# Kernel tuning notes

Measured on AMD Instinct MI355X. Metric: run time of the kernel, lower is better.

Reference implementation:

```python
import jax, jax.numpy as jnp
import numpy as np
from jax import lax

N, H, W, C = 32, 56, 56, 256
K, RATE, STRIDE = 3, 2, 1
BN_EPS = 1e-3  # keras BatchNormalization default epsilon
DN = ('NHWC', 'HWIO', 'NHWC')


def setup_inputs() -> dict:
    key = jax.random.key(0)
    ks = jax.random.split(key, 5)
    return {
        'x': jax.random.normal(ks[0], (N, H, W, C), jnp.float32),
        'dw_kernel': jax.random.normal(ks[1], (K, K, 1, C), jnp.float32) * 0.1,
        'dw_bias': jnp.zeros((C,), jnp.float32),
        'pw_kernel': jax.random.normal(ks[2], (1, 1, C, C), jnp.float32) * 0.05,
        'pw_bias': jnp.zeros((C,), jnp.float32),
        'gamma': jnp.ones((C,), jnp.float32),
        'beta': jnp.zeros((C,), jnp.float32),
        'moving_mean': jax.random.normal(ks[3], (C,), jnp.float32) * 0.1,
        'moving_var': jax.random.uniform(ks[4], (C,), jnp.float32, 0.5, 1.5),
    }


def reference(x, dw_kernel, dw_bias, pw_kernel, pw_bias, gamma, beta, moving_mean, moving_var):
    # ReLU
    h = jax.nn.relu(x)
    # dilated depthwise conv, stride 1, SAME padding (approx-mult LUT modeled as exact MACs)
    h = lax.conv_general_dilated(
        h, dw_kernel, window_strides=(1, 1), padding='SAME',
        rhs_dilation=(RATE, RATE), dimension_numbers=DN,
        feature_group_count=C) + dw_bias
    # pointwise 1x1 conv with stride
    h = lax.conv_general_dilated(
        h, pw_kernel, window_strides=(STRIDE, STRIDE), padding='SAME',
        dimension_numbers=DN) + pw_bias
    # batch norm (inference mode: moving statistics)
    inv = gamma * lax.rsqrt(moving_var + BN_EPS)
    return h * inv + (beta - moving_mean * inv)
```

## Files before the change

kernel.cpp:

```cpp
#include <hip/hip_runtime.h>


typedef _Float16 f16;
typedef _Float16 f16x4 __attribute__((ext_vector_type(4)));
typedef _Float16 f16x8 __attribute__((ext_vector_type(8)));
typedef float    f32x4 __attribute__((ext_vector_type(4)));

constexpr int   N_ = 32, H_ = 56, W_ = 56, C_ = 256;
constexpr int   PIX = 64;
constexpr float BN_EPS = 1e-3f;
constexpr int   WS_BYTES = 4 * 16384 * 2;

struct SM {
    f16   d[PIX * 256];
    f16   w[256 * 64];
    float offC[256];
};

__global__ void prep_w(const float* __restrict__ pwk,
                       const float* __restrict__ gamma,
                       const float* __restrict__ mvar,
                       f16* __restrict__ ws16)
{
    const int co = blockIdx.x;
    const int t  = threadIdx.x;
    const float iv = gamma[co] * rsqrtf(mvar[co] + BN_EPS);
    const float v  = pwk[(size_t)t * C_ + co] * iv;
    const int chunk = t >> 6, k = t & 63;
    ws16[chunk * 16384 + co * 64 + (((k >> 3) ^ (co & 7)) << 3) + (k & 7)] = (f16)v;
}

template <bool FROM_WS>
__global__ __launch_bounds__(256, 2)
void dilconv_mfma(const float* __restrict__ x,
                  const float* __restrict__ dwk,
                  const float* __restrict__ dwb,
                  const float* __restrict__ pwk,
                  const float* __restrict__ pwb,
                  const float* __restrict__ gamma,
                  const float* __restrict__ beta,
                  const float* __restrict__ mmean,
                  const float* __restrict__ mvar,
                  const f16*   __restrict__ wsw,
                  float* __restrict__ out)
{
    extern __shared__ char smem_raw[];
    SM& sm = *reinterpret_cast<SM*>(smem_raw);

    const int tid = threadIdx.x;
    const int bid = (blockIdx.x & 7) * 196 + (blockIdx.x >> 3);
    const int n   = bid / 49;
    const int t   = bid % 49;
    const int h0  = (t / 7) * 8;
    const int w0  = (t % 7) * 8;
    const int l   = tid & 63;
    const int wq  = tid >> 6;

    float invW;
    {
        const float iv = gamma[tid] * rsqrtf(mvar[tid] + BN_EPS);
        invW = iv;
        sm.offC[tid] = pwb[tid] * iv + beta[tid] - mmean[tid] * iv;
    }

    {
        const int c4 = l << 2;
        const int p0 = wq << 4;
        float4 kreg[9];
        #pragma unroll
        for (int kk = 0; kk < 9; ++kk)
            kreg[kk] = *reinterpret_cast<const float4*>(dwk + kk * C_ + c4);
        const float4 bias = *reinterpret_cast<const float4*>(dwb + c4);

        #pragma unroll 2
        for (int pi = 0; pi < 16; ++pi) {
            const int p  = p0 + pi;
            const int ph = h0 + (p >> 3);
            const int pw = w0 + (p & 7);
            float ax = bias.x, ay = bias.y, az = bias.z, aw = bias.w;
            #pragma unroll
            for (int kh = 0; kh < 3; ++kh) {
                const int ih = ph + 2 * kh - 2;
                #pragma unroll
                for (int kw = 0; kw < 3; ++kw) {
                    const int iw = pw + 2 * kw - 2;
                    if ((unsigned)ih < (unsigned)H_ && (unsigned)iw < (unsigned)W_) {
                        const float4 v = *reinterpret_cast<const float4*>(
                            x + (((size_t)(n * H_ + ih) * W_ + iw) * C_) + c4);
                        const float4 kv = kreg[kh * 3 + kw];
                        ax = fmaf(fmaxf(v.x, 0.f), kv.x, ax);
                        ay = fmaf(fmaxf(v.y, 0.f), kv.y, ay);
                        az = fmaf(fmaxf(v.z, 0.f), kv.z, az);
                        aw = fmaf(fmaxf(v.w, 0.f), kv.w, aw);
                    }
                }
            }
            const f16x4 hv = { (f16)ax, (f16)ay, (f16)az, (f16)aw };
            const int idx = p * 256 + ((((c4 >> 3) ^ (p & 7)) << 3) | (c4 & 7));
            *reinterpret_cast<f16x4*>(&sm.d[idx]) = hv;
        }
    }

    f32x4 acc[4][4];
    #pragma unroll
    for (int i = 0; i < 4; ++i)
        #pragma unroll
        for (int j = 0; j < 4; ++j) acc[i][j] = (f32x4){0.f, 0.f, 0.f, 0.f};

    const int arow = l & 15;
    const int koct = l >> 4;

    for (int c = 0; c < 4; ++c) {
        __syncthreads();
        if constexpr (FROM_WS) {
            const float4* wsrc = reinterpret_cast<const float4*>(wsw) + c * 2048;
            #pragma unroll
            for (int i = 0; i < 8; ++i) {
                const int u = i * 256 + tid;
                const float4 v = wsrc[u];
                *reinterpret_cast<float4*>(&sm.w[u * 8]) = v;
            }
        } else {
            const int co = tid;
            const float* wcol = pwk + (size_t)c * 64 * C_ + co;
            #pragma unroll
            for (int g = 0; g < 8; ++g) {
                f16x8 hv;
                #pragma unroll
                for (int j = 0; j < 8; ++j)
                    hv[j] = (f16)(wcol[(g * 8 + j) * C_] * invW);
                *reinterpret_cast<f16x8*>(&sm.w[co * 64 + ((g ^ (co & 7)) << 3)]) = hv;
            }
        }
        __syncthreads();

        #pragma unroll
        for (int ks = 0; ks < 2; ++ks) {
            f16x8 a[4], b[4];
            const int aslot = c * 8 + ks * 4 + koct;
            #pragma unroll
            for (int mt = 0; mt < 4; ++mt) {
                const int row = mt * 16 + arow;
                a[mt] = *reinterpret_cast<const f16x8*>(
                    &sm.d[row * 256 + ((aslot ^ (arow & 7)) << 3)]);
            }
            #pragma unroll
            for (int nt = 0; nt < 4; ++nt) {
                const int co = wq * 64 + nt * 16 + arow;
                b[nt] = *reinterpret_cast<const f16x8*>(
                    &sm.w[co * 64 + (((ks * 4 + koct) ^ (co & 7)) << 3)]);
            }
            #pragma unroll
            for (int mt = 0; mt < 4; ++mt)
                #pragma unroll
                for (int nt = 0; nt < 4; ++nt)
                    acc[mt][nt] = __builtin_amdgcn_mfma_f32_16x16x32_f16(
                        a[mt], b[nt], acc[mt][nt], 0, 0, 0);
        }
    }

    const int prb = (l >> 4) * 4;
    #pragma unroll
    for (int nt = 0; nt < 4; ++nt) {
        const int co  = wq * 64 + nt * 16 + (l & 15);
        const float off = sm.offC[co];
        #pragma unroll
        for (int mt = 0; mt < 4; ++mt) {
            #pragma unroll
            for (int r = 0; r < 4; ++r) {
                const int p  = mt * 16 + prb + r;
                const int oh = h0 + (p >> 3);
                const int ow = w0 + (p & 7);
                out[((size_t)((n * H_ + oh) * W_ + ow)) * C_ + co] = acc[mt][nt][r] + off;
            }
        }
    }
}

extern "C" void kernel_launch(void* const* d_in, const int* in_sizes, int n_in,
                              void* d_out, int out_size, void* d_ws, size_t ws_size,
                              hipStream_t stream) {
    const float* x     = (const float*)d_in[0];
    const float* dwk   = (const float*)d_in[1];
    const float* dwb   = (const float*)d_in[2];
    const float* pwk   = (const float*)d_in[3];
    const float* pwb   = (const float*)d_in[4];
    const float* gam   = (const float*)d_in[5];
    const float* bet   = (const float*)d_in[6];
    const float* mmean = (const float*)d_in[7];
    const float* mvar  = (const float*)d_in[8];
    float* out = (float*)d_out;

    const bool use_ws = (ws_size >= (size_t)WS_BYTES);

    if (use_ws) {
        f16* ws16 = (f16*)d_ws;
        prep_w<<<dim3(256), dim3(256), 0, stream>>>(pwk, gam, mvar, ws16);
        (void)hipFuncSetAttribute(reinterpret_cast<const void*>(&dilconv_mfma<true>),
                                  hipFuncAttributeMaxDynamicSharedMemorySize,
                                  (int)sizeof(SM));
        dilconv_mfma<true><<<dim3(N_ * 49), dim3(256), sizeof(SM), stream>>>(
            x, dwk, dwb, pwk, pwb, gam, bet, mmean, mvar, ws16, out);
    } else {
        (void)hipFuncSetAttribute(reinterpret_cast<const void*>(&dilconv_mfma<false>),
                                  hipFuncAttributeMaxDynamicSharedMemorySize,
                                  (int)sizeof(SM));
        dilconv_mfma<false><<<dim3(N_ * 49), dim3(256), sizeof(SM), stream>>>(
            x, dwk, dwb, pwk, pwb, gam, bet, mmean, mvar, nullptr, out);
    }
}
```

Measured before the change: 347.7 us.

## Restructure fused dilated conv: 512 threads, row-wise depthwise reuse, register-held weights

```diff
diff --git a/kernel.cpp b/kernel.cpp
--- a/kernel.cpp
+++ b/kernel.cpp
@@ -7,171 +7,150 @@
 typedef float    f32x4 __attribute__((ext_vector_type(4)));
 
 constexpr int   N_ = 32, H_ = 56, W_ = 56, C_ = 256;
-constexpr int   PIX = 64;
 constexpr float BN_EPS = 1e-3f;
-constexpr int   WS_BYTES = 4 * 16384 * 2;
 
 struct SM {
-    f16   d[PIX * 256];
-    f16   w[256 * 64];
+    f16   d[64 * 256];
     float offC[256];
 };
 
-__global__ void prep_w(const float* __restrict__ pwk,
-                       const float* __restrict__ gamma,
-                       const float* __restrict__ mvar,
-                       f16* __restrict__ ws16)
+__global__ __launch_bounds__(512, 4)
+void dilconv_fused(const float* __restrict__ x,
+                   const float* __restrict__ dwk,
+                   const float* __restrict__ dwb,
+                   const float* __restrict__ pwk,
+                   const float* __restrict__ pwb,
+                   const float* __restrict__ gamma,
+                   const float* __restrict__ beta,
+                   const float* __restrict__ mmean,
+                   const float* __restrict__ mvar,
+                   float* __restrict__ out)
 {
-    const int co = blockIdx.x;
-    const int t  = threadIdx.x;
-    const float iv = gamma[co] * rsqrtf(mvar[co] + BN_EPS);
-    const float v  = pwk[(size_t)t * C_ + co] * iv;
-    const int chunk = t >> 6, k = t & 63;
-    ws16[chunk * 16384 + co * 64 + (((k >> 3) ^ (co & 7)) << 3) + (k & 7)] = (f16)v;
-}
-
-template <bool FROM_WS>
-__global__ __launch_bounds__(256, 2)
-void dilconv_mfma(const float* __restrict__ x,
-                  const float* __restrict__ dwk,
-                  const float* __restrict__ dwb,
-                  const float* __restrict__ pwk,
-                  const float* __restrict__ pwb,
-                  const float* __restrict__ gamma,
-                  const float* __restrict__ beta,
-                  const float* __restrict__ mmean,
-                  const float* __restrict__ mvar,
-                  const f16*   __restrict__ wsw,
-                  float* __restrict__ out)
-{
-    extern __shared__ char smem_raw[];
-    SM& sm = *reinterpret_cast<SM*>(smem_raw);
+    __shared__ SM sm;
 
     const int tid = threadIdx.x;
+    const int l   = tid & 63;
+    const int wq  = tid >> 6;
     const int bid = (blockIdx.x & 7) * 196 + (blockIdx.x >> 3);
     const int n   = bid / 49;
     const int t   = bid % 49;
     const int h0  = (t / 7) * 8;
     const int w0  = (t % 7) * 8;
-    const int l   = tid & 63;
-    const int wq  = tid >> 6;
 
-    float invW;
-    {
+    if (tid < 256) {
         const float iv = gamma[tid] * rsqrtf(mvar[tid] + BN_EPS);
-        invW = iv;
         sm.offC[tid] = pwb[tid] * iv + beta[tid] - mmean[tid] * iv;
     }
 
     {
+        const int r  = wq;
         const int c4 = l << 2;
-        const int p0 = wq << 4;
-        float4 kreg[9];
+        const int ph = h0 + r;
+        float4 a[8];
+        const float4 bias = *reinterpret_cast<const float4*>(dwb + c4);
         #pragma unroll
-        for (int kk = 0; kk < 9; ++kk)
-            kreg[kk] = *reinterpret_cast<const float4*>(dwk + kk * C_ + c4);
-        const float4 bias = *reinterpret_cast<const float4*>(dwb + c4);
+        for (int ow = 0; ow < 8; ++ow) a[ow] = bias;
 
-        #pragma unroll 2
-        for (int pi = 0; pi < 16; ++pi) {
-            const int p  = p0 + pi;
-            const int ph = h0 + (p >> 3);
-            const int pw = w0 + (p & 7);
-            float ax = bias.x, ay = bias.y, az = bias.z, aw = bias.w;
+        #pragma unroll
+        for (int kh = 0; kh < 3; ++kh) {
+            const int  ih  = ph + 2 * kh - 2;
+            const bool rok = (unsigned)ih < (unsigned)H_;
+            const int  ihc = rok ? ih : 0;
+            const float* xrow = x + ((size_t)(n * H_ + ihc) * W_) * C_ + c4;
+            float4 ld[12];
             #pragma unroll
-            for (int kh = 0; kh < 3; ++kh) {
-                const int ih = ph + 2 * kh - 2;
+            for (int ci = 0; ci < 12; ++ci) {
+                const int  iw  = w0 + ci - 2;
+                const bool ok  = rok && ((unsigned)iw < (unsigned)W_);
+                const int  iwc = ok ? iw : 0;
+                float4 v = *reinterpret_cast<const float4*>(xrow + (size_t)iwc * C_);
+                v.x = ok ? fmaxf(v.x, 0.f) : 0.f;
+                v.y = ok ? fmaxf(v.y, 0.f) : 0.f;
+                v.z = ok ? fmaxf(v.z, 0.f) : 0.f;
+                v.w = ok ? fmaxf(v.w, 0.f) : 0.f;
+                ld[ci] = v;
+            }
+            #pragma unroll
+            for (int kw = 0; kw < 3; ++kw) {
+                const float4 kv = *reinterpret_cast<const float4*>(dwk + (kh * 3 + kw) * C_ + c4);
                 #pragma unroll
-                for (int kw = 0; kw < 3; ++kw) {
-                    const int iw = pw + 2 * kw - 2;
-                    if ((unsigned)ih < (unsigned)H_ && (unsigned)iw < (unsigned)W_) {
-                        const float4 v = *reinterpret_cast<const float4*>(
-                            x + (((size_t)(n * H_ + ih) * W_ + iw) * C_) + c4);
-                        const float4 kv = kreg[kh * 3 + kw];
-                        ax = fmaf(fmaxf(v.x, 0.f), kv.x, ax);
-                        ay = fmaf(fmaxf(v.y, 0.f), kv.y, ay);
-                        az = fmaf(fmaxf(v.z, 0.f), kv.z, az);
-                        aw = fmaf(fmaxf(v.w, 0.f), kv.w, aw);
-                    }
+                for (int ow = 0; ow < 8; ++ow) {
+                    a[ow].x = fmaf(ld[ow + 2 * kw].x, kv.x, a[ow].x);
+                    a[ow].y = fmaf(ld[ow + 2 * kw].y, kv.y, a[ow].y);
+                    a[ow].z = fmaf(ld[ow + 2 * kw].z, kv.z, a[ow].z);
+                    a[ow].w = fmaf(ld[ow + 2 * kw].w, kv.w, a[ow].w);
                 }
             }
-            const f16x4 hv = { (f16)ax, (f16)ay, (f16)az, (f16)aw };
-            const int idx = p * 256 + ((((c4 >> 3) ^ (p & 7)) << 3) | (c4 & 7));
+        }
+        #pragma unroll
+        for (int ow = 0; ow < 8; ++ow) {
+            const int p = r * 8 + ow;
+            const f16x4 hv = { (f16)a[ow].x, (f16)a[ow].y, (f16)a[ow].z, (f16)a[ow].w };
+            const int slot = c4 >> 3;
+            const int idx  = p * 256 + (((slot ^ (p & 7)) << 3) | (c4 & 7));
             *reinterpret_cast<f16x4*>(&sm.d[idx]) = hv;
         }
     }
 
-    f32x4 acc[4][4];
+    __builtin_amdgcn_sched_barrier(0);
+
+    const int arow  = l & 15;
+    const int koctl = l >> 4;
+    f16x8 bw[2][8];
+    #pragma unroll
+    for (int nt = 0; nt < 2; ++nt) {
+        const int co = wq * 32 + nt * 16 + arow;
+        const float iv = gamma[co] * rsqrtf(mvar[co] + BN_EPS);
+        #pragma unroll
+        for (int ks = 0; ks < 8; ++ks) {
+            const int slot = ks * 4 + koctl;
+            const float* wp = pwk + (size_t)(slot * 8) * C_ + co;
+            f16x8 h;
+            #pragma unroll
+            for (int j = 0; j < 8; ++j)
+                h[j] = (f16)(wp[(size_t)j * C_] * iv);
+            bw[nt][ks] = h;
+        }
+    }
+
+    __syncthreads();
+
+    f32x4 acc[4][2];
     #pragma unroll
     for (int i = 0; i < 4; ++i)
         #pragma unroll
-        for (int j = 0; j < 4; ++j) acc[i][j] = (f32x4){0.f, 0.f, 0.f, 0.f};
+        for (int j = 0; j < 2; ++j) acc[i][j] = (f32x4){0.f, 0.f, 0.f, 0.f};
 
-    const int arow = l & 15;
-    const int koct = l >> 4;
-
-    for (int c = 0; c < 4; ++c) {
-        __syncthreads();
-        if constexpr (FROM_WS) {
-            const float4* wsrc = reinterpret_cast<const float4*>(wsw) + c * 2048;
-            #pragma unroll
-            for (int i = 0; i < 8; ++i) {
-                const int u = i * 256 + tid;
-                const float4 v = wsrc[u];
-                *reinterpret_cast<float4*>(&sm.w[u * 8]) = v;
-            }
-        } else {
-            const int co = tid;
-            const float* wcol = pwk + (size_t)c * 64 * C_ + co;
-            #pragma unroll
-            for (int g = 0; g < 8; ++g) {
-                f16x8 hv;
-                #pragma unroll
-                for (int j = 0; j < 8; ++j)
-                    hv[j] = (f16)(wcol[(g * 8 + j) * C_] * invW);
-                *reinterpret_cast<f16x8*>(&sm.w[co * 64 + ((g ^ (co & 7)) << 3)]) = hv;
-            }
+    #pragma unroll
+    for (int ks = 0; ks < 8; ++ks) {
+        const int slot = ks * 4 + koctl;
+        f16x8 af[4];
+        #pragma unroll
+        for (int mt = 0; mt < 4; ++mt) {
+            const int row = mt * 16 + arow;
+            af[mt] = *reinterpret_cast<const f16x8*>(
+                &sm.d[row * 256 + ((slot ^ (row & 7)) << 3)]);
         }
-        __syncthreads();
-
         #pragma unroll
-        for (int ks = 0; ks < 2; ++ks) {
-            f16x8 a[4], b[4];
-            const int aslot = c * 8 + ks * 4 + koct;
-            #pragma unroll
-            for (int mt = 0; mt < 4; ++mt) {
-                const int row = mt * 16 + arow;
-                a[mt] = *reinterpret_cast<const f16x8*>(
-                    &sm.d[row * 256 + ((aslot ^ (arow & 7)) << 3)]);
-            }
-            #pragma unroll
-            for (int nt = 0; nt < 4; ++nt) {
-                const int co = wq * 64 + nt * 16 + arow;
-                b[nt] = *reinterpret_cast<const f16x8*>(
-                    &sm.w[co * 64 + (((ks * 4 + koct) ^ (co & 7)) << 3)]);
-            }
+        for (int nt = 0; nt < 2; ++nt)
             #pragma unroll
             for (int mt = 0; mt < 4; ++mt)
-                #pragma unroll
-                for (int nt = 0; nt < 4; ++nt)
-                    acc[mt][nt] = __builtin_amdgcn_mfma_f32_16x16x32_f16(
-                        a[mt], b[nt], acc[mt][nt], 0, 0, 0);
-        }
+                acc[mt][nt] = __builtin_amdgcn_mfma_f32_16x16x32_f16(
+                    af[mt], bw[nt][ks], acc[mt][nt], 0, 0, 0);
     }
 
-    const int prb = (l >> 4) * 4;
     #pragma unroll
-    for (int nt = 0; nt < 4; ++nt) {
-        const int co  = wq * 64 + nt * 16 + (l & 15);
+    for (int nt = 0; nt < 2; ++nt) {
+        const int   co  = wq * 32 + nt * 16 + arow;
         const float off = sm.offC[co];
         #pragma unroll
         for (int mt = 0; mt < 4; ++mt) {
             #pragma unroll
-            for (int r = 0; r < 4; ++r) {
-                const int p  = mt * 16 + prb + r;
+            for (int rg = 0; rg < 4; ++rg) {
+                const int p  = mt * 16 + koctl * 4 + rg;
                 const int oh = h0 + (p >> 3);
                 const int ow = w0 + (p & 7);
-                out[((size_t)((n * H_ + oh) * W_ + ow)) * C_ + co] = acc[mt][nt][r] + off;
+                out[((size_t)((n * H_ + oh) * W_ + ow)) * C_ + co] = acc[mt][nt][rg] + off;
             }
         }
     }
@@ -191,21 +170,6 @@
     const float* mvar  = (const float*)d_in[8];
     float* out = (float*)d_out;
 
-    const bool use_ws = (ws_size >= (size_t)WS_BYTES);
-
-    if (use_ws) {
-        f16* ws16 = (f16*)d_ws;
-        prep_w<<<dim3(256), dim3(256), 0, stream>>>(pwk, gam, mvar, ws16);
-        (void)hipFuncSetAttribute(reinterpret_cast<const void*>(&dilconv_mfma<true>),
-                                  hipFuncAttributeMaxDynamicSharedMemorySize,
-                                  (int)sizeof(SM));
-        dilconv_mfma<true><<<dim3(N_ * 49), dim3(256), sizeof(SM), stream>>>(
-            x, dwk, dwb, pwk, pwb, gam, bet, mmean, mvar, ws16, out);
-    } else {
-        (void)hipFuncSetAttribute(reinterpret_cast<const void*>(&dilconv_mfma<false>),
-                                  hipFuncAttributeMaxDynamicSharedMemorySize,
-                                  (int)sizeof(SM));
-        dilconv_mfma<false><<<dim3(N_ * 49), dim3(256), sizeof(SM), stream>>>(
-            x, dwk, dwb, pwk, pwb, gam, bet, mmean, mvar, nullptr, out);
-    }
+    dilconv_fused<<<dim3(N_ * 49), dim3(512), 0, stream>>>(
+        x, dwk, dwb, pwk, pwb, gam, bet, mmean, mvar, out);
 }
```

Result: slower. 460.0 us (+32.3%).
